# Performance work log

Measured on AMD Instinct MI355X. Metric: run time of the kernel, lower is better.

## Reference

```python
import jax, jax.numpy as jnp
import numpy as np

N = 20000; E = 120000; D = 1024; H = 8; C = D // H; L = 2; EPS = 1e-5


def setup_inputs() -> dict:
    key = jax.random.key(0)
    ks = jax.random.split(key, 12)
    s = 0.03  # init scale (glorot-ish for d=1024)
    return {
        'x': jax.random.normal(ks[0], (N, D), jnp.float32),
        'edge_index': jax.random.randint(ks[1], (2, E), 0, N),
        'edge_attr': jax.random.randint(ks[2], (E,), 0, 5),
        'node_types': jax.random.randint(ks[3], (N,), 0, 6),
        'node_type_emb': jax.random.normal(ks[4], (6, D), jnp.float32) * s,
        'edge_type_emb': jax.random.normal(ks[5], (5, D), jnp.float32) * s,
        'W_l': jax.random.normal(ks[6], (L, D, D), jnp.float32) * s,
        'b_l': jnp.zeros((L, D), jnp.float32),
        'W_r': jax.random.normal(ks[7], (L, D, D), jnp.float32) * s,
        'b_r': jnp.zeros((L, D), jnp.float32),
        'W_e': jax.random.normal(ks[8], (L, D, D), jnp.float32) * s,
        'att': jax.random.normal(ks[9], (L, H, C), jnp.float32) * s,
        'bias': jnp.zeros((L, D), jnp.float32),
        'ln_gamma': jnp.ones((L, D), jnp.float32),
        'ln_beta': jnp.zeros((L, D), jnp.float32),
        'W_out': jax.random.normal(ks[10], (D, D), jnp.float32) * s,
        'b_out': jnp.zeros((D,), jnp.float32),
        'gate': jnp.array([0.5], jnp.float32),
    }


def _layer_norm(y, g, b):
    mu = y.mean(-1, keepdims=True)
    var = ((y - mu) ** 2).mean(-1, keepdims=True)
    return (y - mu) * jax.lax.rsqrt(var + EPS) * g + b


def reference(x, edge_index, edge_attr, node_types, node_type_emb, edge_type_emb,
              W_l, b_l, W_r, b_r, W_e, att, bias, ln_gamma, ln_beta,
              W_out, b_out, gate):
    src, dst = edge_index[0], edge_index[1]
    e_emb = edge_type_emb[edge_attr]                       # [E, D]
    # PyG add_self_loops(fill_value='mean'): self-loop edge attr = mean of
    # incoming edge attrs (0 if no incoming edges)
    deg = jax.ops.segment_sum(jnp.ones((E,), x.dtype), dst, num_segments=N)
    loop_e = jax.ops.segment_sum(e_emb, dst, num_segments=N) / jnp.maximum(deg, 1.0)[:, None]
    idx = jnp.arange(N, dtype=src.dtype)
    src_a = jnp.concatenate([src, idx])                    # [E+N]
    dst_a = jnp.concatenate([dst, idx])
    e_all = jnp.concatenate([e_emb, loop_e], axis=0)       # [E+N, D]

    h = x + node_type_emb[node_types]
    for l in range(L):
        xl = (h @ W_l[l] + b_l[l]).reshape(N, H, C)        # lin_l (source)
        xr = (h @ W_r[l] + b_r[l]).reshape(N, H, C)        # lin_r (target)
        ee = (e_all @ W_e[l]).reshape(-1, H, C)            # lin_edge (no bias)
        s = jax.nn.leaky_relu(xl[src_a] + xr[dst_a] + ee, 0.2)
        logits = jnp.einsum('ehc,hc->eh', s, att[l])       # [E+N, H]
        # segment softmax over incoming edges per target node
        mx = jax.ops.segment_max(logits, dst_a, num_segments=N)
        ex = jnp.exp(logits - mx[dst_a])
        den = jax.ops.segment_sum(ex, dst_a, num_segments=N)
        alpha = ex / den[dst_a]                            # [E+N, H]
        out = jax.ops.segment_sum(xl[src_a] * alpha[..., None], dst_a,
                                  num_segments=N).reshape(N, D) + bias[l]
        h2 = jax.nn.elu(out)                               # dropout is identity in eval
        h = _layer_norm(h2 + h, ln_gamma[l], ln_beta[l])
    return x + gate * (h @ W_out + b_out)
```

## Files before the change

### kernel.cpp

```cpp
#include <hip/hip_runtime.h>


#define NN 20000
#define NE 120000
#define DD 1024
#define NH 8

typedef __attribute__((ext_vector_type(4))) float f32x4;
typedef __bf16 bf16x8 __attribute__((ext_vector_type(8)));

__device__ __forceinline__ unsigned short f2bf(float f) {
  unsigned int u = __float_as_uint(f);
  u += 0x7FFFu + ((u >> 16) & 1u);
  return (unsigned short)(u >> 16);
}
__device__ __forceinline__ float bf2f(unsigned short u) {
  return __uint_as_float((unsigned int)u << 16);
}
__device__ __forceinline__ void unpack8(uint4 u, float* f) {
  f[0] = __uint_as_float(u.x << 16); f[1] = __uint_as_float(u.x & 0xFFFF0000u);
  f[2] = __uint_as_float(u.y << 16); f[3] = __uint_as_float(u.y & 0xFFFF0000u);
  f[4] = __uint_as_float(u.z << 16); f[5] = __uint_as_float(u.z & 0xFFFF0000u);
  f[6] = __uint_as_float(u.w << 16); f[7] = __uint_as_float(u.w & 0xFFFF0000u);
}


__global__ __launch_bounds__(256) void count_kernel(
    const int* __restrict__ EI, const int* __restrict__ eattr, int* __restrict__ cnt) {
  int e = blockIdx.x * 256 + threadIdx.x;
  if (e < NE) {
    int d = EI[NE + e];
    int t = eattr[e];
    atomicAdd(&cnt[d * 5 + t], 1);
  }
}

__global__ __launch_bounds__(1024) void scan_kernel(
    const int* __restrict__ cnt, int* __restrict__ rowptr, int* __restrict__ cursor) {
  __shared__ int wsum[16];
  __shared__ int carry_s;
  int tid = threadIdx.x, lane = tid & 63, wv = tid >> 6;
  if (tid == 0) carry_s = 0;
  __syncthreads();
  for (int base = 0; base < NN; base += 1024) {
    int n = base + tid;
    int d = 0;
    if (n < NN) {
      const int* c = cnt + n * 5;
      d = c[0] + c[1] + c[2] + c[3] + c[4];
    }
    int v = d;
    #pragma unroll
    for (int off = 1; off < 64; off <<= 1) {
      int t = __shfl_up(v, off);
      if (lane >= off) v += t;
    }
    if (lane == 63) wsum[wv] = v;
    __syncthreads();
    int woff = 0;
    #pragma unroll
    for (int w = 0; w < 16; ++w) if (w < wv) woff += wsum[w];
    int carry = carry_s;
    int excl = carry + woff + v - d;
    if (n < NN) { rowptr[n] = excl; cursor[n] = excl; }
    __syncthreads();
    if (tid == 0) {
      int t = 0;
      #pragma unroll
      for (int w = 0; w < 16; ++w) t += wsum[w];
      carry_s = carry + t;
    }
    __syncthreads();
  }
  if (tid == 0) rowptr[NN] = carry_s;
}

__global__ __launch_bounds__(256) void scatter_kernel(
    const int* __restrict__ EI, int* __restrict__ cursor, int* __restrict__ eids) {
  int e = blockIdx.x * 256 + threadIdx.x;
  if (e < NE) {
    int d = EI[NE + e];
    int pos = atomicAdd(&cursor[d], 1);
    eids[pos] = e;
  }
}


__global__ __launch_bounds__(256) void init_h_kernel(
    const float* __restrict__ x, const int* __restrict__ ntypes,
    const float* __restrict__ ntemb, float* __restrict__ h,
    unsigned short* __restrict__ hb) {
  int idx = blockIdx.x * 256 + threadIdx.x;
  int n = idx >> 8;
  int d4 = idx & 255;
  int t = ntypes[n];
  float4 xv = ((const float4*)x)[idx];
  float4 ev = ((const float4*)ntemb)[t * 256 + d4];
  float4 o;
  o.x = xv.x + ev.x; o.y = xv.y + ev.y; o.z = xv.z + ev.z; o.w = xv.w + ev.w;
  ((float4*)h)[idx] = o;
  ushort4 hv;
  hv.x = f2bf(o.x); hv.y = f2bf(o.y); hv.z = f2bf(o.z); hv.w = f2bf(o.w);
  ((ushort4*)hb)[idx] = hv;
}


__global__ __launch_bounds__(256) void transpose_w_kernel(
    const float* __restrict__ W, unsigned short* __restrict__ WT) {
  __shared__ float tile[32][33];
  int tx = threadIdx.x & 31, ty = threadIdx.x >> 5;
  int bx = blockIdx.x * 32;
  int by = blockIdx.y * 32;
  #pragma unroll
  for (int r = 0; r < 4; ++r)
    tile[ty + r * 8][tx] = W[(size_t)(by + ty + r * 8) * DD + bx + tx];
  __syncthreads();
  #pragma unroll
  for (int r = 0; r < 4; ++r)
    WT[(size_t)(bx + ty + r * 8) * DD + by + tx] = f2bf(tile[tx][ty + r * 8]);
}


__global__ __launch_bounds__(256) void m_kernel(
    const float* __restrict__ ete, const float* __restrict__ We, float* __restrict__ M) {
  __shared__ float red[4][5][64];
  const int jl = threadIdx.x & 63;
  const int kc = threadIdx.x >> 6;
  const int j = blockIdx.x * 64 + jl;
  float acc[5] = {0.f, 0.f, 0.f, 0.f, 0.f};
  const int k0 = kc * 256;
  for (int k = k0; k < k0 + 256; ++k) {
    float w = We[(size_t)k * DD + j];
    #pragma unroll
    for (int t = 0; t < 5; ++t) acc[t] += ete[t * DD + k] * w;
  }
  #pragma unroll
  for (int t = 0; t < 5; ++t) red[kc][t][jl] = acc[t];
  __syncthreads();
  if (threadIdx.x < 64) {
    #pragma unroll
    for (int t = 0; t < 5; ++t)
      M[t * DD + blockIdx.x * 64 + threadIdx.x] =
          red[0][t][threadIdx.x] + red[1][t][threadIdx.x] +
          red[2][t][threadIdx.x] + red[3][t][threadIdx.x];
  }
}


__global__ __launch_bounds__(256) void gemm_bf16(
    const unsigned short* __restrict__ A, const unsigned short* __restrict__ BT,
    const float* __restrict__ bias0, const float* __restrict__ bias1,
    void* __restrict__ C0v, void* __restrict__ C1v,
    const float* __restrict__ resid, const float* __restrict__ gatep,
    int M, int mode) {
  __shared__ unsigned short lsA[128 * 32];
  __shared__ unsigned short lsB[128 * 32];
  const int tid = threadIdx.x;
  const int lane = tid & 63;
  const int wv = tid >> 6;
  const int wm = wv & 1, wn = wv >> 1;

  const int nwg = gridDim.x * gridDim.y;
  const int lid = blockIdx.y * gridDim.x + blockIdx.x;
  const int cpx = nwg >> 3;
  const int swz = (lid & 7) * cpx + (lid >> 3);
  const int bm = swz / gridDim.x, bn = swz % gridDim.x;

  const int row0 = bm * 128, col0 = bn * 128;
  const int l15 = lane & 15, quad = lane >> 4;

  f32x4 acc[4][4];
  #pragma unroll
  for (int mt = 0; mt < 4; ++mt)
    #pragma unroll
    for (int nt = 0; nt < 4; ++nt) {
      f32x4 z = {0.f, 0.f, 0.f, 0.f};
      acc[mt][nt] = z;
    }

  const int r_in = lane >> 2;
  const int kchunk = (lane & 3) * 8;

  for (int kk = 0; kk < DD; kk += 32) {
    #pragma unroll
    for (int j = 0; j < 2; ++j) {
      int r = wv * 32 + j * 16;
      int gr = row0 + r + r_in;
      if (gr > M - 1) gr = M - 1;
      const unsigned short* gpA = A + (size_t)gr * DD + kk + kchunk;
      __builtin_amdgcn_global_load_lds(
          (const __attribute__((address_space(1))) unsigned int*)gpA,
          (__attribute__((address_space(3))) unsigned int*)(lsA + r * 32), 16, 0, 0);
      const unsigned short* gpB = BT + (size_t)(col0 + r + r_in) * DD + kk + kchunk;
      __builtin_amdgcn_global_load_lds(
          (const __attribute__((address_space(1))) unsigned int*)gpB,
          (__attribute__((address_space(3))) unsigned int*)(lsB + r * 32), 16, 0, 0);
    }
    __syncthreads();
    bf16x8 af[4], bfr[4];
    #pragma unroll
    for (int mt = 0; mt < 4; ++mt)
      af[mt] = *(const bf16x8*)(lsA + (wm * 64 + mt * 16 + l15) * 32 + quad * 8);
    #pragma unroll
    for (int nt = 0; nt < 4; ++nt)
      bfr[nt] = *(const bf16x8*)(lsB + (wn * 64 + nt * 16 + l15) * 32 + quad * 8);
    #pragma unroll
    for (int mt = 0; mt < 4; ++mt)
      #pragma unroll
      for (int nt = 0; nt < 4; ++nt)
        acc[mt][nt] = __builtin_amdgcn_mfma_f32_16x16x32_bf16(af[mt], bfr[nt], acc[mt][nt], 0, 0, 0);
    __syncthreads();
  }

  if (mode == 0) {
    unsigned short* Cb = (unsigned short*)(bn < 8 ? C0v : C1v);
    const float* bp = (bn < 8) ? bias0 : bias1;
    int coff = (bn < 8) ? 0 : 1024;
    #pragma unroll
    for (int mt = 0; mt < 4; ++mt) {
      #pragma unroll
      for (int r = 0; r < 4; ++r) {
        int grow = row0 + wm * 64 + mt * 16 + quad * 4 + r;
        if (grow >= M) continue;
        #pragma unroll
        for (int nt = 0; nt < 4; ++nt) {
          int c = col0 - coff + wn * 64 + nt * 16 + l15;
          Cb[(size_t)grow * DD + c] = f2bf(acc[mt][nt][r] + bp[c]);
        }
      }
    }
  } else {
    float* Cp = (float*)C0v;
    float g = gatep[0];
    #pragma unroll
    for (int mt = 0; mt < 4; ++mt) {
      #pragma unroll
      for (int r = 0; r < 4; ++r) {
        int grow = row0 + wm * 64 + mt * 16 + quad * 4 + r;
        if (grow >= M) continue;
        #pragma unroll
        for (int nt = 0; nt < 4; ++nt) {
          int c = col0 + wn * 64 + nt * 16 + l15;
          float v = acc[mt][nt][r] + bias0[c];
          Cp[(size_t)grow * DD + c] = resid[(size_t)grow * DD + c] + g * v;
        }
      }
    }
  }
}


__global__ __launch_bounds__(256) void attn_kernel(
    const unsigned short* __restrict__ xlb, const unsigned short* __restrict__ xrb,
    const int* __restrict__ EI, const int* __restrict__ eattr,
    const int* __restrict__ rowptr, const int* __restrict__ eids,
    const int* __restrict__ cnt, const float* __restrict__ Mbuf,
    const float* __restrict__ attl, const float* __restrict__ biasl,
    const float* __restrict__ gammal, const float* __restrict__ betal,
    float* __restrict__ h, unsigned short* __restrict__ hb) {
  const int lane = threadIdx.x & 63;
  const int wv = threadIdx.x >> 6;
  const int n = blockIdx.x * 4 + wv;
  if (n >= NN) return;
  const int ch = lane * 16;

  float xrf[16], attf[16];
  {
    const uint4* xp = (const uint4*)(xrb + (size_t)n * DD + ch);
    uint4 a = xp[0], b = xp[1];
    unpack8(a, xrf); unpack8(b, xrf + 8);
    const float4* ap = (const float4*)(attl + ch);
    #pragma unroll
    for (int q = 0; q < 4; ++q) {
      float4 t = ap[q];
      attf[q * 4 + 0] = t.x; attf[q * 4 + 1] = t.y;
      attf[q * 4 + 2] = t.z; attf[q * 4 + 3] = t.w;
    }
  }
  float acc[16];
  #pragma unroll
  for (int c = 0; c < 16; ++c) acc[c] = 0.f;
  float den = 0.f;

  const int beg = rowptr[n], end = rowptr[n + 1];
  for (int base = beg; base < end; base += 64) {
    int cc = min(64, end - base);
    int packed = 0;
    if (lane < cc) {
      int eid = eids[base + lane];
      packed = (EI[eid] << 3) | eattr[eid];
    }
    for (int j = 0; j < cc; ++j) {
      int pk = __shfl(packed, j);
      int src = pk >> 3, at = pk & 7;
      const uint4* vp = (const uint4*)(xlb + (size_t)src * DD + ch);
      uint4 v0 = vp[0], v1 = vp[1];
      const float4* mp = (const float4*)(Mbuf + at * DD + ch);
      float vf[16];
      unpack8(v0, vf); unpack8(v1, vf + 8);
      float lg = 0.f;
      #pragma unroll
      for (int q = 0; q < 4; ++q) {
        float4 m = mp[q];
        float s0 = vf[q * 4 + 0] + xrf[q * 4 + 0] + m.x; s0 = fmaxf(s0, 0.2f * s0);
        float s1 = vf[q * 4 + 1] + xrf[q * 4 + 1] + m.y; s1 = fmaxf(s1, 0.2f * s1);
        float s2 = vf[q * 4 + 2] + xrf[q * 4 + 2] + m.z; s2 = fmaxf(s2, 0.2f * s2);
        float s3 = vf[q * 4 + 3] + xrf[q * 4 + 3] + m.w; s3 = fmaxf(s3, 0.2f * s3);
        lg += s0 * attf[q * 4 + 0] + s1 * attf[q * 4 + 1]
            + s2 * attf[q * 4 + 2] + s3 * attf[q * 4 + 3];
      }
      lg += __shfl_xor(lg, 1);
      lg += __shfl_xor(lg, 2);
      lg += __shfl_xor(lg, 4);
      float p = __expf(lg);
      den += p;
      #pragma unroll
      for (int c = 0; c < 16; ++c) acc[c] += p * vf[c];
    }
  }

  {
    const int* c5 = cnt + n * 5;
    int c0 = c5[0], c1 = c5[1], c2 = c5[2], c3 = c5[3], c4 = c5[4];
    float inv = 1.f / fmaxf((float)(c0 + c1 + c2 + c3 + c4), 1.f);
    float w0 = c0 * inv, w1 = c1 * inv, w2 = c2 * inv, w3 = c3 * inv, w4 = c4 * inv;
    const uint4* vp = (const uint4*)(xlb + (size_t)n * DD + ch);
    uint4 v0 = vp[0], v1 = vp[1];
    float vf[16];
    unpack8(v0, vf); unpack8(v1, vf + 8);
    const float* m0 = Mbuf + 0 * DD + ch;
    const float* m1 = Mbuf + 1 * DD + ch;
    const float* m2 = Mbuf + 2 * DD + ch;
    const float* m3 = Mbuf + 3 * DD + ch;
    const float* m4 = Mbuf + 4 * DD + ch;
    float lg = 0.f;
    #pragma unroll
    for (int c = 0; c < 16; ++c) {
      float ee = w0 * m0[c] + w1 * m1[c] + w2 * m2[c] + w3 * m3[c] + w4 * m4[c];
      float s = vf[c] + xrf[c] + ee;
      s = fmaxf(s, 0.2f * s);
      lg += s * attf[c];
    }
    lg += __shfl_xor(lg, 1);
    lg += __shfl_xor(lg, 2);
    lg += __shfl_xor(lg, 4);
    float p = __expf(lg);
    den += p;
    #pragma unroll
    for (int c = 0; c < 16; ++c) acc[c] += p * vf[c];
  }

  float invd = 1.f / den;
  float y[16];
  float s1 = 0.f, s2 = 0.f;
  {
    const float4* bp = (const float4*)(biasl + ch);
    const float4* hp = (const float4*)(h + (size_t)n * DD + ch);
    #pragma unroll
    for (int q = 0; q < 4; ++q) {
      float4 b4 = bp[q];
      float4 h4 = hp[q];
      float o0 = acc[q * 4 + 0] * invd + b4.x;
      float o1 = acc[q * 4 + 1] * invd + b4.y;
      float o2 = acc[q * 4 + 2] * invd + b4.z;
      float o3 = acc[q * 4 + 3] * invd + b4.w;
      o0 = o0 > 0.f ? o0 : (__expf(o0) - 1.f);
      o1 = o1 > 0.f ? o1 : (__expf(o1) - 1.f);
      o2 = o2 > 0.f ? o2 : (__expf(o2) - 1.f);
      o3 = o3 > 0.f ? o3 : (__expf(o3) - 1.f);
      y[q * 4 + 0] = o0 + h4.x; y[q * 4 + 1] = o1 + h4.y;
      y[q * 4 + 2] = o2 + h4.z; y[q * 4 + 3] = o3 + h4.w;
      s1 += y[q * 4 + 0] + y[q * 4 + 1] + y[q * 4 + 2] + y[q * 4 + 3];
      s2 += y[q * 4 + 0] * y[q * 4 + 0] + y[q * 4 + 1] * y[q * 4 + 1]
          + y[q * 4 + 2] * y[q * 4 + 2] + y[q * 4 + 3] * y[q * 4 + 3];
    }
  }
  #pragma unroll
  for (int off = 1; off < 64; off <<= 1) {
    s1 += __shfl_xor(s1, off);
    s2 += __shfl_xor(s2, off);
  }
  float mu = s1 * (1.f / 1024.f);
  float var = s2 * (1.f / 1024.f) - mu * mu;
  float rs = rsqrtf(var + 1e-5f);
  {
    const float4* gp = (const float4*)(gammal + ch);
    const float4* bp = (const float4*)(betal + ch);
    float4* hp = (float4*)(h + (size_t)n * DD + ch);
    uint4* hbp = (uint4*)(hb + (size_t)n * DD + ch);
    uint4 pk0, pk1;
    unsigned int* pk = (unsigned int*)&pk0;
    #pragma unroll
    for (int q = 0; q < 4; ++q) {
      float4 g4 = gp[q];
      float4 b4 = bp[q];
      float4 o4;
      o4.x = (y[q * 4 + 0] - mu) * rs * g4.x + b4.x;
      o4.y = (y[q * 4 + 1] - mu) * rs * g4.y + b4.y;
      o4.z = (y[q * 4 + 2] - mu) * rs * g4.z + b4.z;
      o4.w = (y[q * 4 + 3] - mu) * rs * g4.w + b4.w;
      hp[q] = o4;
      unsigned int lo = (unsigned int)f2bf(o4.x) | ((unsigned int)f2bf(o4.y) << 16);
      unsigned int hi = (unsigned int)f2bf(o4.z) | ((unsigned int)f2bf(o4.w) << 16);
      if (q < 2) { pk[q * 2] = lo; pk[q * 2 + 1] = hi; }
      else {
        unsigned int* pkh = (unsigned int*)&pk1;
        pkh[(q - 2) * 2] = lo; pkh[(q - 2) * 2 + 1] = hi;
      }
    }
    hbp[0] = pk0;
    hbp[1] = pk1;
  }
}


extern "C" void kernel_launch(void* const* d_in, const int* in_sizes, int n_in,
                              void* d_out, int out_size, void* d_ws, size_t ws_size,
                              hipStream_t stream) {
  (void)in_sizes; (void)n_in; (void)out_size; (void)ws_size;
  const float* x      = (const float*)d_in[0];
  const int*   EI     = (const int*)d_in[1];
  const int*   eattr  = (const int*)d_in[2];
  const int*   ntypes = (const int*)d_in[3];
  const float* ntemb  = (const float*)d_in[4];
  const float* etemb  = (const float*)d_in[5];
  const float* W_l    = (const float*)d_in[6];
  const float* b_l    = (const float*)d_in[7];
  const float* W_r    = (const float*)d_in[8];
  const float* b_r    = (const float*)d_in[9];
  const float* W_e    = (const float*)d_in[10];
  const float* att    = (const float*)d_in[11];
  const float* bias   = (const float*)d_in[12];
  const float* gamma  = (const float*)d_in[13];
  const float* beta   = (const float*)d_in[14];
  const float* W_out  = (const float*)d_in[15];
  const float* b_out  = (const float*)d_in[16];
  const float* gate   = (const float*)d_in[17];
  float* out = (float*)d_out;

  char* ws = (char*)d_ws;
  size_t off = 0;
  auto alloc = [&](size_t bytes) {
    char* p = ws + off;
    off = (off + bytes + 255) & ~(size_t)255;
    return p;
  };
  float*          h       = (float*)alloc((size_t)NN * DD * 4);
  unsigned short* hb      = (unsigned short*)alloc((size_t)NN * DD * 2);
  unsigned short* xlb     = (unsigned short*)alloc((size_t)NN * DD * 2);
  unsigned short* xrb     = (unsigned short*)alloc((size_t)NN * DD * 2);
  unsigned short* WTcat   = (unsigned short*)alloc((size_t)2 * DD * DD * 2);
  unsigned short* WT2     = (unsigned short*)alloc((size_t)DD * DD * 2);
  float*          Mbuf    = (float*)alloc((size_t)5 * DD * 4);
  int*            countb  = (int*)alloc((size_t)NN * 5 * 4);
  int*            rowptr  = (int*)alloc((size_t)(NN + 1) * 4);
  int*            cursor  = (int*)alloc((size_t)NN * 4);
  int*            eids    = (int*)alloc((size_t)NE * 4);

  hipMemsetAsync(countb, 0, (size_t)NN * 5 * 4, stream);
  count_kernel<<<(NE + 255) / 256, 256, 0, stream>>>(EI, eattr, countb);
  scan_kernel<<<1, 1024, 0, stream>>>(countb, rowptr, cursor);
  scatter_kernel<<<(NE + 255) / 256, 256, 0, stream>>>(EI, cursor, eids);
  init_h_kernel<<<NN, 256, 0, stream>>>(x, ntypes, ntemb, h, hb);

  dim3 tgrid(DD / 32, DD / 32);
  dim3 ggrid2(16, (NN + 127) / 128);
  dim3 ggrid1(8, (NN + 127) / 128);
  for (int l = 0; l < 2; ++l) {
    transpose_w_kernel<<<tgrid, 256, 0, stream>>>(W_l + (size_t)l * DD * DD, WTcat);
    transpose_w_kernel<<<tgrid, 256, 0, stream>>>(W_r + (size_t)l * DD * DD, WTcat + (size_t)DD * DD);
    m_kernel<<<DD / 64, 256, 0, stream>>>(etemb, W_e + (size_t)l * DD * DD, Mbuf);
    gemm_bf16<<<ggrid2, 256, 0, stream>>>(hb, WTcat, b_l + l * DD, b_r + l * DD,
                                          xlb, xrb, nullptr, nullptr, NN, 0);
    attn_kernel<<<(NN + 3) / 4, 256, 0, stream>>>(xlb, xrb, EI, eattr, rowptr, eids, countb, Mbuf,
                                                  att + l * DD, bias + l * DD,
                                                  gamma + l * DD, beta + l * DD, h, hb);
  }
  transpose_w_kernel<<<tgrid, 256, 0, stream>>>(W_out, WT2);
  gemm_bf16<<<ggrid1, 256, 0, stream>>>(hb, WT2, b_out, nullptr,
                                        out, nullptr, x, gate, NN, 1);
}
```

Baseline: 876.5 us.

## Pre-pack edge src/type in CSR, enlarge attn blocks, skip final fp32 h write

The scatter step now stores a packed (src<<3|type) word per sorted edge, so the attention kernel no longer does the double indirection through edge ids into edge_index and edge_attr. The attention kernel moves to 1024-thread blocks (16 nodes per block) and issues the residual h, count and rowptr loads early to overlap their latency. It also skips writing the fp32 h on the last layer, since only the bf16 copy feeds the output GEMM. The early-exit guard was removed, which relies on NN being divisible by 16. Some dead leftover code remains in the residual loop.

```diff
diff --git a/kernel.cpp b/kernel.cpp
--- a/kernel.cpp
+++ b/kernel.cpp
@@ -76,12 +76,15 @@
 }
 
 __global__ __launch_bounds__(256) void scatter_kernel(
-    const int* __restrict__ EI, int* __restrict__ cursor, int* __restrict__ eids) {
+    const int* __restrict__ EI, const int* __restrict__ eattr,
+    int* __restrict__ cursor, int* __restrict__ epk) {
   int e = blockIdx.x * 256 + threadIdx.x;
   if (e < NE) {
     int d = EI[NE + e];
+    int s = EI[e];
+    int t = eattr[e];
     int pos = atomicAdd(&cursor[d], 1);
-    eids[pos] = e;
+    epk[pos] = (s << 3) | t;
   }
 }
 
@@ -250,19 +253,23 @@
 }
 
 
-__global__ __launch_bounds__(256) void attn_kernel(
+__global__ __launch_bounds__(1024) void attn_kernel(
     const unsigned short* __restrict__ xlb, const unsigned short* __restrict__ xrb,
-    const int* __restrict__ EI, const int* __restrict__ eattr,
-    const int* __restrict__ rowptr, const int* __restrict__ eids,
+    const int* __restrict__ rowptr, const int* __restrict__ epk,
     const int* __restrict__ cnt, const float* __restrict__ Mbuf,
     const float* __restrict__ attl, const float* __restrict__ biasl,
     const float* __restrict__ gammal, const float* __restrict__ betal,
-    float* __restrict__ h, unsigned short* __restrict__ hb) {
+    float* __restrict__ h, unsigned short* __restrict__ hb, int write_h) {
   const int lane = threadIdx.x & 63;
   const int wv = threadIdx.x >> 6;
-  const int n = blockIdx.x * 4 + wv;
-  if (n >= NN) return;
+  const int n = blockIdx.x * 16 + wv;
   const int ch = lane * 16;
+
+  const float4* hp_pre = (const float4*)(h + (size_t)n * DD + ch);
+  float4 h4a = hp_pre[0], h4b = hp_pre[1];
+  const int* c5 = cnt + n * 5;
+  int c0 = c5[0], c1 = c5[1], c2 = c5[2], c3 = c5[3], c4 = c5[4];
+  const int beg = rowptr[n], end = rowptr[n + 1];
 
   float xrf[16], attf[16];
   {
@@ -282,14 +289,10 @@
   for (int c = 0; c < 16; ++c) acc[c] = 0.f;
   float den = 0.f;
 
-  const int beg = rowptr[n], end = rowptr[n + 1];
   for (int base = beg; base < end; base += 64) {
     int cc = min(64, end - base);
     int packed = 0;
-    if (lane < cc) {
-      int eid = eids[base + lane];
-      packed = (EI[eid] << 3) | eattr[eid];
-    }
+    if (lane < cc) packed = epk[base + lane];
     for (int j = 0; j < cc; ++j) {
       int pk = __shfl(packed, j);
       int src = pk >> 3, at = pk & 7;
@@ -320,8 +323,6 @@
   }
 
   {
-    const int* c5 = cnt + n * 5;
-    int c0 = c5[0], c1 = c5[1], c2 = c5[2], c3 = c5[3], c4 = c5[4];
     float inv = 1.f / fmaxf((float)(c0 + c1 + c2 + c3 + c4), 1.f);
     float w0 = c0 * inv, w1 = c1 * inv, w2 = c2 * inv, w3 = c3 * inv, w4 = c4 * inv;
     const uint4* vp = (const uint4*)(xlb + (size_t)n * DD + ch);
@@ -355,11 +356,17 @@
   float s1 = 0.f, s2 = 0.f;
   {
     const float4* bp = (const float4*)(biasl + ch);
-    const float4* hp = (const float4*)(h + (size_t)n * DD + ch);
     #pragma unroll
     for (int q = 0; q < 4; ++q) {
       float4 b4 = bp[q];
-      float4 h4 = hp[q];
+      float4 h4 = (q < 2) ? h4a : h4b;
+      float hx, hy, hz, hw;
+      if (q == 0) { hx = h4a.x; hy = h4a.y; hz = h4a.z; hw = h4a.w; }
+      else if (q == 1) { hx = h4b.x; hy = h4b.y; hz = h4b.z; hw = h4b.w; }
+      else { hx = 0; hy = 0; hz = 0; hw = 0; }
+      (void)h4;
+      if (q >= 2) {
+      }
       float o0 = acc[q * 4 + 0] * invd + b4.x;
       float o1 = acc[q * 4 + 1] * invd + b4.y;
       float o2 = acc[q * 4 + 2] * invd + b4.z;
@@ -368,11 +375,19 @@
       o1 = o1 > 0.f ? o1 : (__expf(o1) - 1.f);
       o2 = o2 > 0.f ? o2 : (__expf(o2) - 1.f);
       o3 = o3 > 0.f ? o3 : (__expf(o3) - 1.f);
-      y[q * 4 + 0] = o0 + h4.x; y[q * 4 + 1] = o1 + h4.y;
-      y[q * 4 + 2] = o2 + h4.z; y[q * 4 + 3] = o3 + h4.w;
-      s1 += y[q * 4 + 0] + y[q * 4 + 1] + y[q * 4 + 2] + y[q * 4 + 3];
-      s2 += y[q * 4 + 0] * y[q * 4 + 0] + y[q * 4 + 1] * y[q * 4 + 1]
-          + y[q * 4 + 2] * y[q * 4 + 2] + y[q * 4 + 3] * y[q * 4 + 3];
+      y[q * 4 + 0] = o0; y[q * 4 + 1] = o1;
+      y[q * 4 + 2] = o2; y[q * 4 + 3] = o3;
+    }
+    const float4* hp = (const float4*)(h + (size_t)n * DD + ch);
+    float4 h4c = hp[2], h4d = hp[3];
+    y[0] += h4a.x;  y[1] += h4a.y;  y[2] += h4a.z;  y[3] += h4a.w;
+    y[4] += h4b.x;  y[5] += h4b.y;  y[6] += h4b.z;  y[7] += h4b.w;
+    y[8] += h4c.x;  y[9] += h4c.y;  y[10] += h4c.z; y[11] += h4c.w;
+    y[12] += h4d.x; y[13] += h4d.y; y[14] += h4d.z; y[15] += h4d.w;
+    #pragma unroll
+    for (int c = 0; c < 16; ++c) {
+      s1 += y[c];
+      s2 += y[c] * y[c];
     }
   }
   #pragma unroll
@@ -399,7 +414,7 @@
       o4.y = (y[q * 4 + 1] - mu) * rs * g4.y + b4.y;
       o4.z = (y[q * 4 + 2] - mu) * rs * g4.z + b4.z;
       o4.w = (y[q * 4 + 3] - mu) * rs * g4.w + b4.w;
-      hp[q] = o4;
+      if (write_h) hp[q] = o4;
       unsigned int lo = (unsigned int)f2bf(o4.x) | ((unsigned int)f2bf(o4.y) << 16);
       unsigned int hi = (unsigned int)f2bf(o4.z) | ((unsigned int)f2bf(o4.w) << 16);
       if (q < 2) { pk[q * 2] = lo; pk[q * 2 + 1] = hi; }
@@ -455,12 +470,12 @@
   int*            countb  = (int*)alloc((size_t)NN * 5 * 4);
   int*            rowptr  = (int*)alloc((size_t)(NN + 1) * 4);
   int*            cursor  = (int*)alloc((size_t)NN * 4);
-  int*            eids    = (int*)alloc((size_t)NE * 4);
+  int*            epk     = (int*)alloc((size_t)NE * 4);
 
   hipMemsetAsync(countb, 0, (size_t)NN * 5 * 4, stream);
   count_kernel<<<(NE + 255) / 256, 256, 0, stream>>>(EI, eattr, countb);
   scan_kernel<<<1, 1024, 0, stream>>>(countb, rowptr, cursor);
-  scatter_kernel<<<(NE + 255) / 256, 256, 0, stream>>>(EI, cursor, eids);
+  scatter_kernel<<<(NE + 255) / 256, 256, 0, stream>>>(EI, eattr, cursor, epk);
   init_h_kernel<<<NN, 256, 0, stream>>>(x, ntypes, ntemb, h, hb);
 
   dim3 tgrid(DD / 32, DD / 32);
@@ -472,9 +487,10 @@
     m_kernel<<<DD / 64, 256, 0, stream>>>(etemb, W_e + (size_t)l * DD * DD, Mbuf);
     gemm_bf16<<<ggrid2, 256, 0, stream>>>(hb, WTcat, b_l + l * DD, b_r + l * DD,
                                           xlb, xrb, nullptr, nullptr, NN, 0);
-    attn_kernel<<<(NN + 3) / 4, 256, 0, stream>>>(xlb, xrb, EI, eattr, rowptr, eids, countb, Mbuf,
-                                                  att + l * DD, bias + l * DD,
-                                                  gamma + l * DD, beta + l * DD, h, hb);
+    attn_kernel<<<NN / 16, 1024, 0, stream>>>(xlb, xrb, rowptr, epk, countb, Mbuf,
+                                              att + l * DD, bias + l * DD,
+                                              gamma + l * DD, beta + l * DD, h, hb,
+                                              l == 0 ? 1 : 0);
   }
   transpose_w_kernel<<<tgrid, 256, 0, stream>>>(W_out, WT2);
   gemm_bf16<<<ggrid1, 256, 0, stream>>>(hb, WT2, b_out, nullptr,
```

After: 936.5 us. 1.07x slower.
